# Kernel tuning notes

Hardware: AMD Instinct MI355X
Metric: run time of the kernel (lower is better)

## Reference

```python
import jax, jax.numpy as jnp
import numpy as np

DIM = 512
HEADS = 8
DIM_HEAD = 64
HIDDEN = HEADS * DIM_HEAD  # 512
SCALE = DIM_HEAD ** -0.5


def setup_inputs() -> dict:
    key = jax.random.key(0)
    k1, k2, k3 = jax.random.split(key, 3)
    x = jax.random.normal(k1, (4, 2048, DIM), dtype=jnp.float32)
    # torch Linear weight convention: [out_features, in_features], y = x @ W.T
    W_qkv = jax.random.normal(k2, (3 * HIDDEN, DIM), dtype=jnp.float32) * (DIM ** -0.5)
    W_out = jax.random.normal(k3, (DIM, HIDDEN), dtype=jnp.float32) * (HIDDEN ** -0.5)
    return {"x": x, "W_qkv": W_qkv, "W_out": W_out}


def reference(x, W_qkv, W_out):
    b, n, c = x.shape
    qkv = jnp.einsum('bnc,oc->bno', x, W_qkv)  # [b, n, 3*hidden]
    q, k, v = jnp.split(qkv, 3, axis=-1)
    # rearrange 'b n (h c) -> b h c n'
    def to_heads(t):
        return jnp.transpose(t.reshape(b, n, HEADS, DIM_HEAD), (0, 2, 3, 1))
    q, k, v = to_heads(q), to_heads(k), to_heads(v)
    q = q * SCALE
    sim = jnp.einsum('bhcn,bhcj->bhnj', q, k)  # [b, h, n, n]
    attn = jax.nn.softmax(sim, axis=-1)
    out = jnp.einsum('bhnj,bhdj->bhnd', attn, v)  # [b, h, n, d]
    out = jnp.transpose(out, (0, 2, 1, 3)).reshape(b, n, HIDDEN)  # 'b h n d -> b n (h d)'
    return jnp.einsum('bnh,oh->bno', out, W_out)
```

## Files before the change

kernel.cpp:

```cpp
#include <hip/hip_runtime.h>


typedef unsigned short u16;
typedef __attribute__((ext_vector_type(8))) short s16x8;
typedef __attribute__((ext_vector_type(4))) float f32x4;
typedef __attribute__((ext_vector_type(16))) float f32x16;

__device__ __forceinline__ u16 f2bf(float f) {
  unsigned int u = __float_as_uint(f);
  u = (u + 0x7fffu + ((u >> 16) & 1u)) >> 16;
  return (u16)u;
}

__global__ __launch_bounds__(256) void cvt4(const float* __restrict__ in,
                                            u16* __restrict__ out, int n4) {
  int i = blockIdx.x * 256 + threadIdx.x;
  if (i >= n4) return;
  float4 f = ((const float4*)in)[i];
  uint2 o;
  o.x = (unsigned)f2bf(f.x) | ((unsigned)f2bf(f.y) << 16);
  o.y = (unsigned)f2bf(f.z) | ((unsigned)f2bf(f.w) << 16);
  ((uint2*)out)[i] = o;
}

template <int MODE>
__global__ __launch_bounds__(256) void gemm_bt(
    const u16* __restrict__ A, const u16* __restrict__ B,
    float* __restrict__ Cf,
    u16* __restrict__ Qp, u16* __restrict__ Kp, u16* __restrict__ Vp) {
  constexpr int K = 512;
  __shared__ u16 As[64][40];
  __shared__ u16 Bs[64][40];
  const int bm0 = blockIdx.x * 64;
  const int bn0 = blockIdx.y * 64;
  const int t = threadIdx.x;
  const int wave = t >> 6, lane = t & 63;
  const int quad = lane >> 4, l16 = lane & 15;
  const int wm = (wave & 1) * 32, wn = (wave >> 1) * 32;
  const int srow = t >> 2, scol = (t & 3) * 8;

  f32x4 acc[2][2] = {};

  for (int k0 = 0; k0 < K; k0 += 32) {
    __syncthreads();
    s16x8 av = *(const s16x8*)(A + (size_t)(bm0 + srow) * K + k0 + scol);
    s16x8 bv = *(const s16x8*)(B + (size_t)(bn0 + srow) * K + k0 + scol);
    *(s16x8*)(&As[srow][scol]) = av;
    *(s16x8*)(&Bs[srow][scol]) = bv;
    __syncthreads();
    s16x8 af[2], bf[2];
#pragma unroll
    for (int i = 0; i < 2; i++) af[i] = *(const s16x8*)(&As[wm + i * 16 + l16][quad * 8]);
#pragma unroll
    for (int j = 0; j < 2; j++) bf[j] = *(const s16x8*)(&Bs[wn + j * 16 + l16][quad * 8]);
#pragma unroll
    for (int i = 0; i < 2; i++)
#pragma unroll
      for (int j = 0; j < 2; j++)
        acc[i][j] = __builtin_amdgcn_mfma_f32_16x16x32_bf16(af[i], bf[j], acc[i][j], 0, 0, 0);
  }

#pragma unroll
  for (int i = 0; i < 2; i++)
#pragma unroll
    for (int j = 0; j < 2; j++)
#pragma unroll
      for (int r = 0; r < 4; r++) {
        int m = bm0 + wm + i * 16 + quad * 4 + r;
        int n = bn0 + wn + j * 16 + l16;
        float v = acc[i][j][r];
        if constexpr (MODE == 1) {
          Cf[(size_t)m * 512 + n] = v;
        } else {
          int part = n >> 9;
          int oin = n & 511;
          int head = oin >> 6, dh = oin & 63;
          int bb = m >> 11, tok = m & 2047;
          if (part == 0) {
            size_t idx = ((size_t)(bb * 8 + head) * 2048 + tok) * 64 + dh;
            Qp[idx] = f2bf(v * 0.18033688011112042f);
          } else if (part == 1) {
            size_t idx = ((size_t)(bb * 8 + head) * 2048 + tok) * 64 + dh;
            Kp[idx] = f2bf(v);
          } else {
            size_t idx = ((size_t)(bb * 8 + head) * 64 + dh) * 2048 + tok;
            Vp[idx] = f2bf(v);
          }
        }
      }
}

__global__ __launch_bounds__(256) void attn_kernel(
    const u16* __restrict__ Qg, const u16* __restrict__ Kg,
    const u16* __restrict__ Vtg, u16* __restrict__ Og) {
  __shared__ u16 Qs[64][72];
  __shared__ u16 Ks[64][72];
  __shared__ u16 Vt[64][72];
  __shared__ u16 Ps[64][72];
  __shared__ float Ls[2][64];
  const int bh = blockIdx.y;
  const int q0 = blockIdx.x * 64;
  const u16* Qh = Qg + (size_t)bh * 2048 * 64;
  const u16* Kh = Kg + (size_t)bh * 2048 * 64;
  const u16* Vh = Vtg + (size_t)bh * 64 * 2048;
  const int t = threadIdx.x, lane = t & 63, wave = t >> 6;
  const int wq = wave & 1, wk = wave >> 1;
  const int l32 = lane & 31, half = lane >> 5;
  const int srow = t >> 2, scolb = (t & 3) * 8;

#pragma unroll
  for (int p = 0; p < 2; p++) {
    int col = scolb + p * 32;
    *(s16x8*)(&Qs[srow][col]) = *(const s16x8*)(Qh + (size_t)(q0 + srow) * 64 + col);
  }
  __syncthreads();
  s16x8 aq[4];
#pragma unroll
  for (int ks = 0; ks < 4; ks++)
    aq[ks] = *(const s16x8*)(&Qs[wq * 32 + l32][ks * 16 + half * 8]);

  f32x16 o = {};
  float l_part[16];
#pragma unroll
  for (int r = 0; r < 16; r++) l_part[r] = 0.f;

  for (int j0 = 0; j0 < 2048; j0 += 64) {
    __syncthreads();
#pragma unroll
    for (int p = 0; p < 2; p++) {
      int col = scolb + p * 32;
      *(s16x8*)(&Ks[srow][col]) = *(const s16x8*)(Kh + (size_t)(j0 + srow) * 64 + col);
      *(s16x8*)(&Vt[srow][col]) = *(const s16x8*)(Vh + (size_t)srow * 2048 + j0 + col);
    }
    __syncthreads();

    f32x16 s = {};
#pragma unroll
    for (int ks = 0; ks < 4; ks++) {
      s16x8 bk = *(const s16x8*)(&Ks[wk * 32 + l32][ks * 16 + half * 8]);
      s = __builtin_amdgcn_mfma_f32_32x32x16_bf16(aq[ks], bk, s, 0, 0, 0);
    }

#pragma unroll
    for (int r = 0; r < 16; r++) {
      float p = __builtin_amdgcn_exp2f(s[r]);
      unsigned u = __float_as_uint(p);
      l_part[r] += __uint_as_float(u & 0xffff0000u);
      int row = (r & 3) + 8 * (r >> 2) + 4 * half + wq * 32;
      Ps[row][wk * 32 + l32] = (u16)(u >> 16);
    }
    __syncthreads();

#pragma unroll
    for (int ks = 0; ks < 4; ks++) {
      s16x8 ap = *(const s16x8*)(&Ps[wq * 32 + l32][ks * 16 + half * 8]);
      s16x8 bv = *(const s16x8*)(&Vt[wk * 32 + l32][ks * 16 + half * 8]);
      o = __builtin_amdgcn_mfma_f32_32x32x16_bf16(ap, bv, o, 0, 0, 0);
    }
  }

#pragma unroll
  for (int r = 0; r < 16; r++) {
#pragma unroll
    for (int msk = 1; msk < 32; msk <<= 1)
      l_part[r] += __shfl_xor(l_part[r], msk, 64);
  }
  if (l32 == 0) {
#pragma unroll
    for (int r = 0; r < 16; r++) {
      int rowl = (r & 3) + 8 * (r >> 2) + 4 * half;
      Ls[wk][wq * 32 + rowl] = l_part[r];
    }
  }
  __syncthreads();

  const int bb = bh >> 3, h = bh & 7;
#pragma unroll
  for (int r = 0; r < 16; r++) {
    int rowl = (r & 3) + 8 * (r >> 2) + 4 * half;
    float l = Ls[0][wq * 32 + rowl] + Ls[1][wq * 32 + rowl];
    float val = o[r] * __builtin_amdgcn_rcpf(l);
    int row = q0 + wq * 32 + rowl;
    Og[((size_t)bb * 2048 + row) * 512 + h * 64 + wk * 32 + l32] = f2bf(val);
  }
}

extern "C" void kernel_launch(void* const* d_in, const int* in_sizes, int n_in,
                              void* d_out, int out_size, void* d_ws, size_t ws_size,
                              hipStream_t stream) {
  const float* x    = (const float*)d_in[0];
  const float* Wqkv = (const float*)d_in[1];
  const float* Wout = (const float*)d_in[2];
  float* y = (float*)d_out;

  char* ws = (char*)d_ws;
  size_t off = 0;
  auto alloc = [&](size_t bytes) {
    void* p = ws + off;
    off += (bytes + 255) & ~(size_t)255;
    return p;
  };
  u16* xb    = (u16*)alloc((size_t)8192 * 512 * 2);
  u16* wqkvb = (u16*)alloc((size_t)1536 * 512 * 2);
  u16* woutb = (u16*)alloc((size_t)512 * 512 * 2);
  u16* Qw    = (u16*)alloc((size_t)32 * 2048 * 64 * 2);
  u16* Kw    = (u16*)alloc((size_t)32 * 2048 * 64 * 2);
  u16* Vw    = (u16*)alloc((size_t)32 * 2048 * 64 * 2);
  u16* Ow    = (u16*)alloc((size_t)8192 * 512 * 2);
  if (off > ws_size) return;

  cvt4<<<4096, 256, 0, stream>>>(x, xb, 8192 * 512 / 4);
  cvt4<<<768, 256, 0, stream>>>(Wqkv, wqkvb, 1536 * 512 / 4);
  cvt4<<<256, 256, 0, stream>>>(Wout, woutb, 512 * 512 / 4);

  gemm_bt<0><<<dim3(128, 24), 256, 0, stream>>>(xb, wqkvb, nullptr, Qw, Kw, Vw);
  attn_kernel<<<dim3(32, 32), 256, 0, stream>>>(Qw, Kw, Vw, Ow);
  gemm_bt<1><<<dim3(128, 8), 256, 0, stream>>>(Ow, woutb, y, nullptr, nullptr, nullptr);
}
```

Before: 186.6 us.

## Use larger swizzled GEMM tiles with direct-to-LDS loads and packed P stores

Replaces the 64x64 GEMM with 128xBN tiles, K-step 64, an XOR-swizzled LDS layout, and global_load_lds direct-to-shared copies, which raises operand reuse and cuts register staging and bank conflicts. In attention, adjacent lanes exchange bf16 probabilities with shuffles so each lane writes packed 32-bit words to LDS instead of 16-bit scalar stores. This costs more registers per GEMM thread and fewer blocks, which may hurt occupancy on the smaller output projection.

```diff
diff --git a/kernel.cpp b/kernel.cpp
--- a/kernel.cpp
+++ b/kernel.cpp
@@ -10,6 +10,12 @@
   unsigned int u = __float_as_uint(f);
   u = (u + 0x7fffu + ((u >> 16) & 1u)) >> 16;
   return (u16)u;
+}
+
+__device__ __forceinline__ void gload16(const u16* g, u16* lds_base) {
+  __builtin_amdgcn_global_load_lds(
+      (const __attribute__((address_space(1))) unsigned int*)g,
+      (__attribute__((address_space(3))) unsigned int*)lds_base, 16, 0, 0);
 }
 
 __global__ __launch_bounds__(256) void cvt4(const float* __restrict__ in,
@@ -23,47 +29,64 @@
   ((uint2*)out)[i] = o;
 }
 
-template <int MODE>
-__global__ __launch_bounds__(256) void gemm_bt(
+template <int BN, int MODE>
+__global__ __launch_bounds__(256) void gemm128(
     const u16* __restrict__ A, const u16* __restrict__ B,
     float* __restrict__ Cf,
     u16* __restrict__ Qp, u16* __restrict__ Kp, u16* __restrict__ Vp) {
   constexpr int K = 512;
-  __shared__ u16 As[64][40];
-  __shared__ u16 Bs[64][40];
-  const int bm0 = blockIdx.x * 64;
-  const int bn0 = blockIdx.y * 64;
-  const int t = threadIdx.x;
-  const int wave = t >> 6, lane = t & 63;
+  constexpr int JN = BN / 32;
+  __shared__ u16 As[128 * 64];
+  __shared__ u16 Bs[BN * 64];
+  const int bm0 = blockIdx.x * 128, bn0 = blockIdx.y * BN;
+  const int t = threadIdx.x, wave = t >> 6, lane = t & 63;
   const int quad = lane >> 4, l16 = lane & 15;
-  const int wm = (wave & 1) * 32, wn = (wave >> 1) * 32;
-  const int srow = t >> 2, scol = (t & 3) * 8;
-
-  f32x4 acc[2][2] = {};
-
-  for (int k0 = 0; k0 < K; k0 += 32) {
-    __syncthreads();
-    s16x8 av = *(const s16x8*)(A + (size_t)(bm0 + srow) * K + k0 + scol);
-    s16x8 bv = *(const s16x8*)(B + (size_t)(bn0 + srow) * K + k0 + scol);
-    *(s16x8*)(&As[srow][scol]) = av;
-    *(s16x8*)(&Bs[srow][scol]) = bv;
-    __syncthreads();
-    s16x8 af[2], bf[2];
-#pragma unroll
-    for (int i = 0; i < 2; i++) af[i] = *(const s16x8*)(&As[wm + i * 16 + l16][quad * 8]);
-#pragma unroll
-    for (int j = 0; j < 2; j++) bf[j] = *(const s16x8*)(&Bs[wn + j * 16 + l16][quad * 8]);
-#pragma unroll
-    for (int i = 0; i < 2; i++)
-#pragma unroll
-      for (int j = 0; j < 2; j++)
-        acc[i][j] = __builtin_amdgcn_mfma_f32_16x16x32_bf16(af[i], bf[j], acc[i][j], 0, 0, 0);
-  }
-
-#pragma unroll
-  for (int i = 0; i < 2; i++)
-#pragma unroll
-    for (int j = 0; j < 2; j++)
+  const int wm = (wave & 1) * 64, wn = (wave >> 1) * (BN / 2);
+  const int lr = lane >> 3, lc = lane & 7;
+  const int swz = lc ^ lr;
+
+  f32x4 acc[4][JN] = {};
+
+  for (int k0 = 0; k0 < K; k0 += 64) {
+    __syncthreads();
+#pragma unroll
+    for (int a = 0; a < 4; a++) {
+      int r = wave * 32 + a * 8 + lr;
+      gload16(A + (size_t)(bm0 + r) * K + k0 + swz * 8,
+              &As[(wave * 32 + a * 8) * 64]);
+    }
+#pragma unroll
+    for (int b = 0; b < BN / 32; b++) {
+      int r = wave * (BN / 4) + b * 8 + lr;
+      gload16(B + (size_t)(bn0 + r) * K + k0 + swz * 8,
+              &Bs[(wave * (BN / 4) + b * 8) * 64]);
+    }
+    __syncthreads();
+#pragma unroll
+    for (int ks = 0; ks < 2; ks++) {
+      s16x8 af[4], bf[JN];
+#pragma unroll
+      for (int i = 0; i < 4; i++) {
+        int m = wm + i * 16 + l16;
+        af[i] = *(const s16x8*)(&As[m * 64 + (((ks * 4 + quad) ^ (m & 7)) * 8)]);
+      }
+#pragma unroll
+      for (int j = 0; j < JN; j++) {
+        int n = wn + j * 16 + l16;
+        bf[j] = *(const s16x8*)(&Bs[n * 64 + (((ks * 4 + quad) ^ (n & 7)) * 8)]);
+      }
+#pragma unroll
+      for (int i = 0; i < 4; i++)
+#pragma unroll
+        for (int j = 0; j < JN; j++)
+          acc[i][j] = __builtin_amdgcn_mfma_f32_16x16x32_bf16(af[i], bf[j], acc[i][j], 0, 0, 0);
+    }
+  }
+
+#pragma unroll
+  for (int i = 0; i < 4; i++)
+#pragma unroll
+    for (int j = 0; j < JN; j++)
 #pragma unroll
       for (int r = 0; r < 4; r++) {
         int m = bm0 + wm + i * 16 + quad * 4 + r;
@@ -141,13 +164,25 @@
       s = __builtin_amdgcn_mfma_f32_32x32x16_bf16(aq[ks], bk, s, 0, 0, 0);
     }
 
+    unsigned pb[16];
 #pragma unroll
     for (int r = 0; r < 16; r++) {
       float p = __builtin_amdgcn_exp2f(s[r]);
       unsigned u = __float_as_uint(p);
       l_part[r] += __uint_as_float(u & 0xffff0000u);
+      pb[r] = u >> 16;
+    }
+    const int odd = l32 & 1;
+    const int colb = wk * 32 + (l32 & ~1);
+#pragma unroll
+    for (int rp = 0; rp < 8; rp++) {
+      unsigned v0 = pb[2 * rp], v1 = pb[2 * rp + 1];
+      unsigned t0 = __shfl_xor(v0, 1, 64);
+      unsigned t1 = __shfl_xor(v1, 1, 64);
+      int r = 2 * rp + odd;
       int row = (r & 3) + 8 * (r >> 2) + 4 * half + wq * 32;
-      Ps[row][wk * 32 + l32] = (u16)(u >> 16);
+      unsigned packed = odd ? (t1 | (v1 << 16)) : (v0 | (t0 << 16));
+      *(unsigned*)(&Ps[row][colb]) = packed;
     }
     __syncthreads();
 
@@ -213,7 +248,7 @@
   cvt4<<<768, 256, 0, stream>>>(Wqkv, wqkvb, 1536 * 512 / 4);
   cvt4<<<256, 256, 0, stream>>>(Wout, woutb, 512 * 512 / 4);
 
-  gemm_bt<0><<<dim3(128, 24), 256, 0, stream>>>(xb, wqkvb, nullptr, Qw, Kw, Vw);
+  gemm128<128, 0><<<dim3(64, 12), 256, 0, stream>>>(xb, wqkvb, nullptr, Qw, Kw, Vw);
   attn_kernel<<<dim3(32, 32), 256, 0, stream>>>(Qw, Kw, Vw, Ow);
-  gemm_bt<1><<<dim3(128, 8), 256, 0, stream>>>(Ow, woutb, y, nullptr, nullptr, nullptr);
-}
+  gemm128<64, 1><<<dim3(64, 8), 256, 0, stream>>>(Ow, woutb, y, nullptr, nullptr, nullptr);
+}
```

New measurement: 197.4 us. +5.8%, slower.
